# Kernel tuning notes

Measured on AMD Instinct MI355X. Metric: run time of the kernel, lower is better.

## Reference

```python
import jax, jax.numpy as jnp
import numpy as np

N_NODES = 50000
N_EDGES = 800000
D_IN = 128
D_OUT = 128
BN_EPS = 1e-5


def setup_inputs() -> dict:
    key = jax.random.key(0)
    ks = jax.random.split(key, 6)
    feat = jax.random.normal(ks[0], (N_NODES, D_IN), dtype=jnp.float32)
    src = jax.random.randint(ks[1], (N_EDGES,), 0, N_NODES, dtype=jnp.int32)
    dst = jax.random.randint(ks[2], (N_EDGES,), 0, N_NODES, dtype=jnp.int32)
    W = jax.random.normal(ks[3], (D_IN, D_OUT), dtype=jnp.float32) * (1.0 / np.sqrt(D_IN))
    b = jnp.zeros((D_OUT,), dtype=jnp.float32)
    a1 = jnp.full((1,), 0.25, dtype=jnp.float32)  # PReLU inside GraphConv
    gamma = jnp.ones((D_OUT,), dtype=jnp.float32)
    beta = jnp.zeros((D_OUT,), dtype=jnp.float32)
    a2 = jnp.full((1,), 0.25, dtype=jnp.float32)  # PReLU after BN
    return {"feat": feat, "src": src, "dst": dst, "W": W, "b": b,
            "a1": a1, "gamma": gamma, "beta": beta, "a2": a2}


def _prelu(x, a):
    return jnp.where(x >= 0, x, a * x)


def reference(feat, src, dst, W, b, a1, gamma, beta, a2):
    # Degrees (DGL clamps to min 1 to avoid inf norms)
    ones_e = jnp.ones((src.shape[0],), dtype=feat.dtype)
    out_deg = jnp.clip(jax.ops.segment_sum(ones_e, src, num_segments=N_NODES), 1.0)
    in_deg = jnp.clip(jax.ops.segment_sum(ones_e, dst, num_segments=N_NODES), 1.0)
    norm_src = jax.lax.rsqrt(out_deg)[:, None]   # [N,1]
    norm_dst = jax.lax.rsqrt(in_deg)[:, None]    # [N,1]

    # Dropout (eval mode -> identity), source normalization, projection
    h = (feat * norm_src) @ W                    # [N, D_OUT]
    # Gather-scatter neighbor aggregation (SpMM): sum over incoming edges
    msg = h[src]                                 # [E, D_OUT]
    agg = jax.ops.segment_sum(msg, dst, num_segments=N_NODES)  # [N, D_OUT]
    h = agg * norm_dst + b                       # dst normalization + bias
    h = _prelu(h, a1)                            # GraphConv activation

    # BatchNorm1d over node dimension (training-mode batch stats, biased var)
    mean = jnp.mean(h, axis=0)
    var = jnp.mean((h - mean) ** 2, axis=0)
    h = (h - mean) * jax.lax.rsqrt(var + BN_EPS) * gamma + beta

    return _prelu(h, a2)
```

## Files before the change

kernel.cpp:

```cpp
#include <hip/hip_runtime.h>
#include <hip/hip_bf16.h>

#define N_NODES 50000
#define N_EDGES 800000
#define D 128
#define BN_EPS 1e-5f
#define ELLW 64
#define PROJ_LDK 136
#define SPMM_BLOCKS 1564

#define BINS 128
#define BIN_RANGE 391
#define BINCAP 8192
#define A_EPT 13
#define A_BLOCKS 256

typedef __attribute__((ext_vector_type(8))) short bf16x8;
typedef __attribute__((ext_vector_type(4))) float f32x4;

__device__ inline float bf_lo(unsigned u) { union { unsigned x; float f; } c; c.x = u << 16; return c.f; }
__device__ inline float bf_hi(unsigned u) { union { unsigned x; float f; } c; c.x = u & 0xffff0000u; return c.f; }
__device__ inline unsigned short f2bf(float f) {
    union { float f; unsigned u; } c; c.f = f;
    unsigned u = c.u;
    u += 0x7fff + ((u >> 16) & 1);
    return (unsigned short)(u >> 16);
}
__device__ inline unsigned pack2bf(float a, float b) {
    return (unsigned)f2bf(a) | ((unsigned)f2bf(b) << 16);
}

__global__ __launch_bounds__(256) void bucket_kernel(const int* __restrict__ src,
                                                     const int* __restrict__ dst,
                                                     int* __restrict__ gdbase,
                                                     int* __restrict__ gsbase,
                                                     unsigned* __restrict__ dbkt,
                                                     unsigned short* __restrict__ sbkt) {
    __shared__ int dcnt[BINS], scnt[BINS], dbase[BINS], sbase[BINS];
    const int tid = threadIdx.x;
    if (tid < BINS) { dcnt[tid] = 0; scnt[tid] = 0; }
    __syncthreads();

    const int e0 = blockIdx.x * (256 * A_EPT) + tid;
    int s[A_EPT], t[A_EPT], dr[A_EPT], sr[A_EPT];
    #pragma unroll
    for (int k = 0; k < A_EPT; ++k) {
        int e = e0 + k * 256;
        if (e < N_EDGES) { s[k] = src[e]; t[k] = dst[e]; }
        else             { s[k] = -1;     t[k] = -1;     }
    }
    #pragma unroll
    for (int k = 0; k < A_EPT; ++k) {
        if (t[k] >= 0) dr[k] = atomicAdd(&dcnt[t[k] / BIN_RANGE], 1);
        if (s[k] >= 0) sr[k] = atomicAdd(&scnt[s[k] / BIN_RANGE], 1);
    }
    __syncthreads();
    if (tid < BINS) {
        dbase[tid] = atomicAdd(&gdbase[tid], dcnt[tid]);
        sbase[tid] = atomicAdd(&gsbase[tid], scnt[tid]);
    }
    __syncthreads();
    #pragma unroll
    for (int k = 0; k < A_EPT; ++k) {
        if (t[k] >= 0) {
            int b = t[k] / BIN_RANGE;
            int p = dbase[b] + dr[k];
            if (p < BINCAP)
                dbkt[b * BINCAP + p] = (unsigned)s[k] | ((unsigned)(t[k] - b * BIN_RANGE) << 16);
        }
        if (s[k] >= 0) {
            int b = s[k] / BIN_RANGE;
            int p = sbase[b] + sr[k];
            if (p < BINCAP)
                sbkt[b * BINCAP + p] = (unsigned short)(s[k] - b * BIN_RANGE);
        }
    }
}

__global__ __launch_bounds__(1024) void build_kernel(const int* __restrict__ gdbase,
                                                     const int* __restrict__ gsbase,
                                                     const unsigned* __restrict__ dbkt,
                                                     const unsigned short* __restrict__ sbkt,
                                                     unsigned short* __restrict__ ell,
                                                     int* __restrict__ cnt,
                                                     int* __restrict__ deg_out) {
    __shared__ int hist[BIN_RANGE];
    const int tid = threadIdx.x;
    const int bin = blockIdx.x & (BINS - 1);
    const int lo  = bin * BIN_RANGE;

    for (int i = tid; i < BIN_RANGE; i += 1024) hist[i] = 0;
    __syncthreads();

    if (blockIdx.x < BINS) {
        int count = gdbase[bin]; if (count > BINCAP) count = BINCAP;
        const unsigned* bkt = dbkt + bin * BINCAP;
        int i = tid;
        for (; i + 3072 < count; i += 4096) {
            unsigned e0 = bkt[i], e1 = bkt[i + 1024], e2 = bkt[i + 2048], e3 = bkt[i + 3072];
            int r0 = atomicAdd(&hist[e0 >> 16], 1);
            int r1 = atomicAdd(&hist[e1 >> 16], 1);
            int r2 = atomicAdd(&hist[e2 >> 16], 1);
            int r3 = atomicAdd(&hist[e3 >> 16], 1);
            if (r0 < ELLW) ell[(size_t)(lo + (e0 >> 16)) * ELLW + r0] = (unsigned short)(e0 & 0xffffu);
            if (r1 < ELLW) ell[(size_t)(lo + (e1 >> 16)) * ELLW + r1] = (unsigned short)(e1 & 0xffffu);
            if (r2 < ELLW) ell[(size_t)(lo + (e2 >> 16)) * ELLW + r2] = (unsigned short)(e2 & 0xffffu);
            if (r3 < ELLW) ell[(size_t)(lo + (e3 >> 16)) * ELLW + r3] = (unsigned short)(e3 & 0xffffu);
        }
        for (; i < count; i += 1024) {
            unsigned e = bkt[i];
            int r = atomicAdd(&hist[e >> 16], 1);
            if (r < ELLW) ell[(size_t)(lo + (e >> 16)) * ELLW + r] = (unsigned short)(e & 0xffffu);
        }
        __syncthreads();
        for (int j = tid; j < BIN_RANGE; j += 1024)
            if (lo + j < N_NODES) cnt[lo + j] = hist[j];
    } else {
        int count = gsbase[bin]; if (count > BINCAP) count = BINCAP;
        const unsigned short* bkt = sbkt + bin * BINCAP;
        int i = tid;
        for (; i + 3072 < count; i += 4096) {
            int v0 = bkt[i], v1 = bkt[i + 1024], v2 = bkt[i + 2048], v3 = bkt[i + 3072];
            atomicAdd(&hist[v0], 1); atomicAdd(&hist[v1], 1);
            atomicAdd(&hist[v2], 1); atomicAdd(&hist[v3], 1);
        }
        for (; i < count; i += 1024) atomicAdd(&hist[bkt[i]], 1);
        __syncthreads();
        for (int j = tid; j < BIN_RANGE; j += 1024)
            if (lo + j < N_NODES) deg_out[lo + j] = hist[j];
    }
}

__global__ __launch_bounds__(256, 2) void proj_kernel(const float* __restrict__ feat,
                                                      const float* __restrict__ W,
                                                      const int* __restrict__ deg_out,
                                                      unsigned short* __restrict__ h) {
    __shared__ unsigned short Wt[D * PROJ_LDK];

    const int tid  = threadIdx.x;
    const int wave = tid >> 6;
    const int lane = tid & 63;
    const int quad = lane >> 4;
    const int l16  = lane & 15;

    for (int idx = tid; idx < D * D; idx += 256) {
        int k = idx >> 7, d = idx & 127;
        Wt[d * PROJ_LDK + k] = f2bf(W[idx]);
    }
    __syncthreads();

    bf16x8 breg[8][4];
    #pragma unroll
    for (int dt = 0; dt < 8; ++dt)
        #pragma unroll
        for (int kk = 0; kk < 4; ++kk)
            breg[dt][kk] = *(const bf16x8*)&Wt[(dt * 16 + l16) * PROJ_LDK + kk * 32 + quad * 8];

    const int n_tiles = (N_NODES + 63) / 64;
    for (int tile = blockIdx.x; tile < n_tiles; tile += gridDim.x) {
        const int base = tile * 64;
        const int arow = base + wave * 16 + l16;
        const bool rok = arow < N_NODES;
        float nm;
        {
            int dg = rok ? deg_out[arow] : 1;
            nm = rsqrtf((float)(dg < 1 ? 1 : dg));
        }

        f32x4 acc[8];
        #pragma unroll
        for (int dt = 0; dt < 8; ++dt) acc[dt] = (f32x4){0.f, 0.f, 0.f, 0.f};

        #pragma unroll
        for (int kk = 0; kk < 4; ++kk) {
            bf16x8 af;
            if (rok) {
                const float4* fp = (const float4*)(feat + (size_t)arow * D + kk * 32 + quad * 8);
                float4 f0 = fp[0], f1 = fp[1];
                af[0] = (short)f2bf(f0.x * nm); af[1] = (short)f2bf(f0.y * nm);
                af[2] = (short)f2bf(f0.z * nm); af[3] = (short)f2bf(f0.w * nm);
                af[4] = (short)f2bf(f1.x * nm); af[5] = (short)f2bf(f1.y * nm);
                af[6] = (short)f2bf(f1.z * nm); af[7] = (short)f2bf(f1.w * nm);
            } else {
                af = (bf16x8){0, 0, 0, 0, 0, 0, 0, 0};
            }
            #pragma unroll
            for (int dt = 0; dt < 8; ++dt)
                acc[dt] = __builtin_amdgcn_mfma_f32_16x16x32_bf16(af, breg[dt][kk], acc[dt], 0, 0, 0);
        }

        #pragma unroll
        for (int dt = 0; dt < 8; ++dt) {
            #pragma unroll
            for (int r = 0; r < 4; ++r) {
                int n = base + wave * 16 + quad * 4 + r;
                if (n < N_NODES)
                    h[(size_t)n * D + dt * 16 + l16] = f2bf(acc[dt][r]);
            }
        }
    }
}

#define ACCA(v) { accA[0] += bf_lo((v).x); accA[1] += bf_hi((v).x); \
                  accA[2] += bf_lo((v).y); accA[3] += bf_hi((v).y); \
                  accA[4] += bf_lo((v).z); accA[5] += bf_hi((v).z); \
                  accA[6] += bf_lo((v).w); accA[7] += bf_hi((v).w); }
#define ACCB(v) { accB[0] += bf_lo((v).x); accB[1] += bf_hi((v).x); \
                  accB[2] += bf_lo((v).y); accB[3] += bf_hi((v).y); \
                  accB[4] += bf_lo((v).z); accB[5] += bf_hi((v).z); \
                  accB[6] += bf_lo((v).w); accB[7] += bf_hi((v).w); }
#define GA(sid) { uint4 vv = *(const uint4*)(h + (size_t)(sid) * D + coff); ACCA(vv); }
#define GB(sid) { uint4 vv = *(const uint4*)(h + (size_t)(sid) * D + coff); ACCB(vv); }

__global__ __launch_bounds__(256) void spmm_kernel(const int* __restrict__ cnt,
                                                   const unsigned short* __restrict__ ell,
                                                   const unsigned short* __restrict__ h,
                                                   const float* __restrict__ b,
                                                   const float* __restrict__ a1,
                                                   unsigned short* __restrict__ h2,
                                                   float* __restrict__ bn_sum,
                                                   float* __restrict__ bn_sumsq) {
    const int tid  = threadIdx.x;
    const int l16  = tid & 15;
    const int slot = (blockIdx.x * 256 + tid) >> 4;
    const float alpha = a1[0];
    const size_t coff = (size_t)l16 * 8;

    float bias[8];
    #pragma unroll
    for (int j = 0; j < 8; ++j) bias[j] = b[l16 * 8 + j];

    float lsum[8] = {0,0,0,0,0,0,0,0};
    float lsq[8]  = {0,0,0,0,0,0,0,0};

    if (slot < N_NODES / 2) {
        const int n0 = slot * 2;
        const int n1 = n0 + 1;
        int dgA = cnt[n0], dgB = cnt[n1];
        int endA = (dgA < ELLW) ? dgA : ELLW;
        int endB = (dgB < ELLW) ? dgB : ELLW;
        const unsigned short* rowA = ell + (size_t)n0 * ELLW;
        const unsigned short* rowB = ell + (size_t)n1 * ELLW;

        float accA[8] = {0,0,0,0,0,0,0,0};
        float accB[8] = {0,0,0,0,0,0,0,0};
        int iA = 0, iB = 0;

        while (iA + 8 <= endA && iB + 8 <= endB) {
            uint4 ra = *(const uint4*)(rowA + iA);
            uint4 rb = *(const uint4*)(rowB + iB);
            GA(ra.x & 0xffff); GA(ra.x >> 16);
            GA(ra.y & 0xffff); GA(ra.y >> 16);
            GA(ra.z & 0xffff); GA(ra.z >> 16);
            GA(ra.w & 0xffff); GA(ra.w >> 16);
            GB(rb.x & 0xffff); GB(rb.x >> 16);
            GB(rb.y & 0xffff); GB(rb.y >> 16);
            GB(rb.z & 0xffff); GB(rb.z >> 16);
            GB(rb.w & 0xffff); GB(rb.w >> 16);
            iA += 8; iB += 8;
        }
        for (; iA + 8 <= endA; iA += 8) {
            uint4 ra = *(const uint4*)(rowA + iA);
            GA(ra.x & 0xffff); GA(ra.x >> 16);
            GA(ra.y & 0xffff); GA(ra.y >> 16);
            GA(ra.z & 0xffff); GA(ra.z >> 16);
            GA(ra.w & 0xffff); GA(ra.w >> 16);
        }
        for (; iB + 8 <= endB; iB += 8) {
            uint4 rb = *(const uint4*)(rowB + iB);
            GB(rb.x & 0xffff); GB(rb.x >> 16);
            GB(rb.y & 0xffff); GB(rb.y >> 16);
            GB(rb.z & 0xffff); GB(rb.z >> 16);
            GB(rb.w & 0xffff); GB(rb.w >> 16);
        }
        for (; iA < endA; ++iA) { GA(rowA[iA]); }
        for (; iB < endB; ++iB) { GB(rowB[iB]); }

        float ndA = rsqrtf((float)(dgA < 1 ? 1 : dgA));
        float ndB = rsqrtf((float)(dgB < 1 ? 1 : dgB));
        float xA[8], xB[8];
        #pragma unroll
        for (int j = 0; j < 8; ++j) {
            float va = accA[j] * ndA + bias[j];
            va = (va >= 0.f) ? va : alpha * va;
            xA[j] = va; lsum[j] += va; lsq[j] += va * va;
            float vb = accB[j] * ndB + bias[j];
            vb = (vb >= 0.f) ? vb : alpha * vb;
            xB[j] = vb; lsum[j] += vb; lsq[j] += vb * vb;
        }
        uint4 oA, oB;
        oA.x = pack2bf(xA[0], xA[1]); oA.y = pack2bf(xA[2], xA[3]);
        oA.z = pack2bf(xA[4], xA[5]); oA.w = pack2bf(xA[6], xA[7]);
        oB.x = pack2bf(xB[0], xB[1]); oB.y = pack2bf(xB[2], xB[3]);
        oB.z = pack2bf(xB[4], xB[5]); oB.w = pack2bf(xB[6], xB[7]);
        *(uint4*)(h2 + (size_t)n0 * D + coff) = oA;
        *(uint4*)(h2 + (size_t)n1 * D + coff) = oB;
    }

    #pragma unroll
    for (int j = 0; j < 8; ++j) {
        lsum[j] += __shfl_xor(lsum[j], 16);
        lsum[j] += __shfl_xor(lsum[j], 32);
        lsq[j]  += __shfl_xor(lsq[j], 16);
        lsq[j]  += __shfl_xor(lsq[j], 32);
    }
    __shared__ float red[4][256];
    const int wave = tid >> 6;
    const int lane = tid & 63;
    if (lane < 16) {
        #pragma unroll
        for (int j = 0; j < 8; ++j) {
            red[wave][l16 * 16 + j]     = lsum[j];
            red[wave][l16 * 16 + 8 + j] = lsq[j];
        }
    }
    __syncthreads();
    {
        float tot = red[0][tid] + red[1][tid] + red[2][tid] + red[3][tid];
        int l = tid >> 4;
        int v = tid & 15;
        int dim = l * 8 + (v & 7);
        int rep = (blockIdx.x & 3) * D;
        if (v < 8) atomicAdd(&bn_sum[rep + dim], tot);
        else       atomicAdd(&bn_sumsq[rep + dim], tot);
    }
}

__global__ __launch_bounds__(256) void final_kernel(const unsigned short* __restrict__ h2,
                                                    const float* __restrict__ bn_sum,
                                                    const float* __restrict__ bn_sumsq,
                                                    const float* __restrict__ gamma,
                                                    const float* __restrict__ beta,
                                                    const float* __restrict__ a2,
                                                    float* __restrict__ out) {
    int i8 = blockIdx.x * 256 + threadIdx.x;
    if (i8 < N_NODES * D / 8) {
        int dbase = (i8 * 8) & (D - 1);
        const float invN = 1.0f / (float)N_NODES;
        const float alpha = a2[0];
        uint4 v = ((const uint4*)h2)[i8];
        float xv[8] = { bf_lo(v.x), bf_hi(v.x), bf_lo(v.y), bf_hi(v.y),
                        bf_lo(v.z), bf_hi(v.z), bf_lo(v.w), bf_hi(v.w) };
        float r[8];
        #pragma unroll
        for (int j = 0; j < 8; ++j) {
            int d = dbase + j;
            float sm = bn_sum[d] + bn_sum[D + d] + bn_sum[2 * D + d] + bn_sum[3 * D + d];
            float sq = bn_sumsq[d] + bn_sumsq[D + d] + bn_sumsq[2 * D + d] + bn_sumsq[3 * D + d];
            float mean = sm * invN;
            float var  = sq * invN - mean * mean;
            float inv  = rsqrtf(var + BN_EPS);
            float t = (xv[j] - mean) * inv * gamma[d] + beta[d];
            r[j] = (t >= 0.f) ? t : alpha * t;
        }
        float4* po = (float4*)(out + (size_t)i8 * 8);
        po[0] = make_float4(r[0], r[1], r[2], r[3]);
        po[1] = make_float4(r[4], r[5], r[6], r[7]);
    }
}

extern "C" void kernel_launch(void* const* d_in, const int* in_sizes, int n_in,
                              void* d_out, int out_size, void* d_ws, size_t ws_size,
                              hipStream_t stream) {
    const float* feat  = (const float*)d_in[0];
    const int*   src   = (const int*)  d_in[1];
    const int*   dst   = (const int*)  d_in[2];
    const float* W     = (const float*)d_in[3];
    const float* b     = (const float*)d_in[4];
    const float* a1    = (const float*)d_in[5];
    const float* gamma = (const float*)d_in[6];
    const float* beta  = (const float*)d_in[7];
    const float* a2    = (const float*)d_in[8];
    float* out = (float*)d_out;

    char* ws = (char*)d_ws;
    int*            gdbase    = (int*)(ws + 0);
    int*            gsbase    = (int*)(ws + 512);
    float*          bn_sum    = (float*)(ws + 1024);
    float*          bn_sumsq  = (float*)(ws + 3072);
    int*            cnt       = (int*)(ws + 5120);
    int*            deg_out_p = (int*)(ws + 205120);
    unsigned short* ell       = (unsigned short*)(ws + 405120);
    unsigned short* h         = (unsigned short*)(ws + 6805120);
    unsigned short* h2        = (unsigned short*)(ws + 19605120);
    unsigned*       dbkt      = (unsigned*)(ws + 32405120);
    unsigned short* sbkt      = (unsigned short*)(ws + 36599424);

    hipMemsetAsync(ws, 0, 5120, stream);

    bucket_kernel<<<A_BLOCKS, 256, 0, stream>>>(src, dst, gdbase, gsbase, dbkt, sbkt);

    build_kernel<<<2 * BINS, 1024, 0, stream>>>(gdbase, gsbase, dbkt, sbkt,
                                                ell, cnt, deg_out_p);

    proj_kernel<<<782, 256, 0, stream>>>(feat, W, deg_out_p, h);

    spmm_kernel<<<SPMM_BLOCKS, 256, 0, stream>>>(cnt, ell, h, b, a1, h2, bn_sum, bn_sumsq);

    final_kernel<<<(N_NODES * D / 8 + 255) / 256, 256, 0, stream>>>(h2, bn_sum, bn_sumsq,
                                                                    gamma, beta, a2, out);
}
```

Baseline: 183.2 us.

## Fuse projection into bucketing kernel and apply source norm inside SpMM gather

The projection no longer needs out-degrees, because the per-source normalization is now applied as a scalar per gathered row inside the SpMM. That lets the projection GEMM run in the same launch as edge bucketing, with extra blocks handling the projection tiles, which removes one kernel launch and lets the two independent stages overlap. build_kernel now writes rsqrt(out-degree) floats instead of raw degree ints. Software bf16 rounding is replaced with the v_cvt_pk_bf16_f32 instruction. In exchange, the SpMM does an extra scalar load per edge, feat is converted to bf16 before scaling, which changes rounding slightly, and each projection block now restages W for only a single tile.

```diff
diff --git a/kernel.cpp b/kernel.cpp
--- a/kernel.cpp
+++ b/kernel.cpp
@@ -8,6 +8,7 @@
 #define ELLW 64
 #define PROJ_LDK 136
 #define SPMM_BLOCKS 1564
+#define PROJ_TILES 782
 
 #define BINS 128
 #define BIN_RANGE 391
@@ -26,53 +27,125 @@
     u += 0x7fff + ((u >> 16) & 1);
     return (unsigned short)(u >> 16);
 }
-__device__ inline unsigned pack2bf(float a, float b) {
-    return (unsigned)f2bf(a) | ((unsigned)f2bf(b) << 16);
-}
-
-__global__ __launch_bounds__(256) void bucket_kernel(const int* __restrict__ src,
-                                                     const int* __restrict__ dst,
-                                                     int* __restrict__ gdbase,
-                                                     int* __restrict__ gsbase,
-                                                     unsigned* __restrict__ dbkt,
-                                                     unsigned short* __restrict__ sbkt) {
+__device__ inline unsigned cvt_pk_bf16(float lo, float hi) {
+    unsigned r;
+    asm("v_cvt_pk_bf16_f32 %0, %1, %2" : "=v"(r) : "v"(lo), "v"(hi));
+    return r;
+}
+
+__global__ __launch_bounds__(256, 2) void bucket_proj_kernel(
+        const int* __restrict__ src,
+        const int* __restrict__ dst,
+        int* __restrict__ gdbase,
+        int* __restrict__ gsbase,
+        unsigned* __restrict__ dbkt,
+        unsigned short* __restrict__ sbkt,
+        const float* __restrict__ feat,
+        const float* __restrict__ W,
+        unsigned short* __restrict__ h) {
     __shared__ int dcnt[BINS], scnt[BINS], dbase[BINS], sbase[BINS];
+    __shared__ unsigned short Wt[D * PROJ_LDK];
+
     const int tid = threadIdx.x;
-    if (tid < BINS) { dcnt[tid] = 0; scnt[tid] = 0; }
-    __syncthreads();
-
-    const int e0 = blockIdx.x * (256 * A_EPT) + tid;
-    int s[A_EPT], t[A_EPT], dr[A_EPT], sr[A_EPT];
-    #pragma unroll
-    for (int k = 0; k < A_EPT; ++k) {
-        int e = e0 + k * 256;
-        if (e < N_EDGES) { s[k] = src[e]; t[k] = dst[e]; }
-        else             { s[k] = -1;     t[k] = -1;     }
-    }
-    #pragma unroll
-    for (int k = 0; k < A_EPT; ++k) {
-        if (t[k] >= 0) dr[k] = atomicAdd(&dcnt[t[k] / BIN_RANGE], 1);
-        if (s[k] >= 0) sr[k] = atomicAdd(&scnt[s[k] / BIN_RANGE], 1);
-    }
-    __syncthreads();
-    if (tid < BINS) {
-        dbase[tid] = atomicAdd(&gdbase[tid], dcnt[tid]);
-        sbase[tid] = atomicAdd(&gsbase[tid], scnt[tid]);
-    }
-    __syncthreads();
-    #pragma unroll
-    for (int k = 0; k < A_EPT; ++k) {
-        if (t[k] >= 0) {
-            int b = t[k] / BIN_RANGE;
-            int p = dbase[b] + dr[k];
-            if (p < BINCAP)
-                dbkt[b * BINCAP + p] = (unsigned)s[k] | ((unsigned)(t[k] - b * BIN_RANGE) << 16);
-        }
-        if (s[k] >= 0) {
-            int b = s[k] / BIN_RANGE;
-            int p = sbase[b] + sr[k];
-            if (p < BINCAP)
-                sbkt[b * BINCAP + p] = (unsigned short)(s[k] - b * BIN_RANGE);
+
+    if (blockIdx.x < A_BLOCKS) {
+        if (tid < BINS) { dcnt[tid] = 0; scnt[tid] = 0; }
+        __syncthreads();
+
+        const int e0 = blockIdx.x * (256 * A_EPT) + tid;
+        int s[A_EPT], t[A_EPT], dr[A_EPT], sr[A_EPT];
+        #pragma unroll
+        for (int k = 0; k < A_EPT; ++k) {
+            int e = e0 + k * 256;
+            if (e < N_EDGES) { s[k] = src[e]; t[k] = dst[e]; }
+            else             { s[k] = -1;     t[k] = -1;     }
+        }
+        #pragma unroll
+        for (int k = 0; k < A_EPT; ++k) {
+            if (t[k] >= 0) dr[k] = atomicAdd(&dcnt[t[k] / BIN_RANGE], 1);
+            if (s[k] >= 0) sr[k] = atomicAdd(&scnt[s[k] / BIN_RANGE], 1);
+        }
+        __syncthreads();
+        if (tid < BINS) {
+            dbase[tid] = atomicAdd(&gdbase[tid], dcnt[tid]);
+            sbase[tid] = atomicAdd(&gsbase[tid], scnt[tid]);
+        }
+        __syncthreads();
+        #pragma unroll
+        for (int k = 0; k < A_EPT; ++k) {
+            if (t[k] >= 0) {
+                int bb = t[k] / BIN_RANGE;
+                int p = dbase[bb] + dr[k];
+                if (p < BINCAP)
+                    dbkt[bb * BINCAP + p] = (unsigned)s[k] | ((unsigned)(t[k] - bb * BIN_RANGE) << 16);
+            }
+            if (s[k] >= 0) {
+                int bb = s[k] / BIN_RANGE;
+                int p = sbase[bb] + sr[k];
+                if (p < BINCAP)
+                    sbkt[bb * BINCAP + p] = (unsigned short)(s[k] - bb * BIN_RANGE);
+            }
+        }
+    } else {
+        const int tile = blockIdx.x - A_BLOCKS;
+        const int wave = tid >> 6;
+        const int lane = tid & 63;
+        const int quad = lane >> 4;
+        const int l16  = lane & 15;
+
+        for (int idx = tid; idx < D * D; idx += 256) {
+            int k = idx >> 7, d = idx & 127;
+            Wt[d * PROJ_LDK + k] = f2bf(W[idx]);
+        }
+        __syncthreads();
+
+        bf16x8 breg[8][4];
+        #pragma unroll
+        for (int dt = 0; dt < 8; ++dt)
+            #pragma unroll
+            for (int kk = 0; kk < 4; ++kk)
+                breg[dt][kk] = *(const bf16x8*)&Wt[(dt * 16 + l16) * PROJ_LDK + kk * 32 + quad * 8];
+
+        const int base = tile * 64;
+        const int arow = base + wave * 16 + l16;
+        const bool rok = arow < N_NODES;
+
+        f32x4 acc[8];
+        #pragma unroll
+        for (int dt = 0; dt < 8; ++dt) acc[dt] = (f32x4){0.f, 0.f, 0.f, 0.f};
+
+        #pragma unroll
+        for (int kk = 0; kk < 4; ++kk) {
+            bf16x8 af = (bf16x8){0, 0, 0, 0, 0, 0, 0, 0};
+            if (rok) {
+                const float4* fp = (const float4*)(feat + (size_t)arow * D + kk * 32 + quad * 8);
+                float4 f0 = fp[0], f1 = fp[1];
+                unsigned u0 = cvt_pk_bf16(f0.x, f0.y);
+                unsigned u1 = cvt_pk_bf16(f0.z, f0.w);
+                unsigned u2 = cvt_pk_bf16(f1.x, f1.y);
+                unsigned u3 = cvt_pk_bf16(f1.z, f1.w);
+                af[0] = (short)(u0 & 0xffff); af[1] = (short)(u0 >> 16);
+                af[2] = (short)(u1 & 0xffff); af[3] = (short)(u1 >> 16);
+                af[4] = (short)(u2 & 0xffff); af[5] = (short)(u2 >> 16);
+                af[6] = (short)(u3 & 0xffff); af[7] = (short)(u3 >> 16);
+            }
+            #pragma unroll
+            for (int dt = 0; dt < 8; ++dt)
+                acc[dt] = __builtin_amdgcn_mfma_f32_16x16x32_bf16(af, breg[dt][kk], acc[dt], 0, 0, 0);
+        }
+
+        #pragma unroll
+        for (int r = 0; r < 4; ++r) {
+            int n = base + wave * 16 + quad * 4 + r;
+            if (n < N_NODES) {
+                unsigned short* hp = h + (size_t)n * D + l16;
+                #pragma unroll
+                for (int dt = 0; dt < 8; dt += 2) {
+                    unsigned pk = cvt_pk_bf16(acc[dt][r], acc[dt + 1][r]);
+                    hp[dt * 16]       = (unsigned short)(pk & 0xffff);
+                    hp[(dt + 1) * 16] = (unsigned short)(pk >> 16);
+                }
+            }
         }
     }
 }
@@ -83,7 +156,7 @@
                                                      const unsigned short* __restrict__ sbkt,
                                                      unsigned short* __restrict__ ell,
                                                      int* __restrict__ cnt,
-                                                     int* __restrict__ deg_out) {
+                                                     float* __restrict__ nsrc) {
     __shared__ int hist[BIN_RANGE];
     const int tid = threadIdx.x;
     const int bin = blockIdx.x & (BINS - 1);
@@ -127,92 +200,28 @@
         for (; i < count; i += 1024) atomicAdd(&hist[bkt[i]], 1);
         __syncthreads();
         for (int j = tid; j < BIN_RANGE; j += 1024)
-            if (lo + j < N_NODES) deg_out[lo + j] = hist[j];
-    }
-}
-
-__global__ __launch_bounds__(256, 2) void proj_kernel(const float* __restrict__ feat,
-                                                      const float* __restrict__ W,
-                                                      const int* __restrict__ deg_out,
-                                                      unsigned short* __restrict__ h) {
-    __shared__ unsigned short Wt[D * PROJ_LDK];
-
-    const int tid  = threadIdx.x;
-    const int wave = tid >> 6;
-    const int lane = tid & 63;
-    const int quad = lane >> 4;
-    const int l16  = lane & 15;
-
-    for (int idx = tid; idx < D * D; idx += 256) {
-        int k = idx >> 7, d = idx & 127;
-        Wt[d * PROJ_LDK + k] = f2bf(W[idx]);
-    }
-    __syncthreads();
-
-    bf16x8 breg[8][4];
-    #pragma unroll
-    for (int dt = 0; dt < 8; ++dt)
-        #pragma unroll
-        for (int kk = 0; kk < 4; ++kk)
-            breg[dt][kk] = *(const bf16x8*)&Wt[(dt * 16 + l16) * PROJ_LDK + kk * 32 + quad * 8];
-
-    const int n_tiles = (N_NODES + 63) / 64;
-    for (int tile = blockIdx.x; tile < n_tiles; tile += gridDim.x) {
-        const int base = tile * 64;
-        const int arow = base + wave * 16 + l16;
-        const bool rok = arow < N_NODES;
-        float nm;
-        {
-            int dg = rok ? deg_out[arow] : 1;
-            nm = rsqrtf((float)(dg < 1 ? 1 : dg));
-        }
-
-        f32x4 acc[8];
-        #pragma unroll
-        for (int dt = 0; dt < 8; ++dt) acc[dt] = (f32x4){0.f, 0.f, 0.f, 0.f};
-
-        #pragma unroll
-        for (int kk = 0; kk < 4; ++kk) {
-            bf16x8 af;
-            if (rok) {
-                const float4* fp = (const float4*)(feat + (size_t)arow * D + kk * 32 + quad * 8);
-                float4 f0 = fp[0], f1 = fp[1];
-                af[0] = (short)f2bf(f0.x * nm); af[1] = (short)f2bf(f0.y * nm);
-                af[2] = (short)f2bf(f0.z * nm); af[3] = (short)f2bf(f0.w * nm);
-                af[4] = (short)f2bf(f1.x * nm); af[5] = (short)f2bf(f1.y * nm);
-                af[6] = (short)f2bf(f1.z * nm); af[7] = (short)f2bf(f1.w * nm);
-            } else {
-                af = (bf16x8){0, 0, 0, 0, 0, 0, 0, 0};
+            if (lo + j < N_NODES) {
+                int dg = hist[j];
+                nsrc[lo + j] = rsqrtf((float)(dg < 1 ? 1 : dg));
             }
-            #pragma unroll
-            for (int dt = 0; dt < 8; ++dt)
-                acc[dt] = __builtin_amdgcn_mfma_f32_16x16x32_bf16(af, breg[dt][kk], acc[dt], 0, 0, 0);
-        }
-
-        #pragma unroll
-        for (int dt = 0; dt < 8; ++dt) {
-            #pragma unroll
-            for (int r = 0; r < 4; ++r) {
-                int n = base + wave * 16 + quad * 4 + r;
-                if (n < N_NODES)
-                    h[(size_t)n * D + dt * 16 + l16] = f2bf(acc[dt][r]);
-            }
-        }
-    }
-}
-
-#define ACCA(v) { accA[0] += bf_lo((v).x); accA[1] += bf_hi((v).x); \
-                  accA[2] += bf_lo((v).y); accA[3] += bf_hi((v).y); \
-                  accA[4] += bf_lo((v).z); accA[5] += bf_hi((v).z); \
-                  accA[6] += bf_lo((v).w); accA[7] += bf_hi((v).w); }
-#define ACCB(v) { accB[0] += bf_lo((v).x); accB[1] += bf_hi((v).x); \
-                  accB[2] += bf_lo((v).y); accB[3] += bf_hi((v).y); \
-                  accB[4] += bf_lo((v).z); accB[5] += bf_hi((v).z); \
-                  accB[6] += bf_lo((v).w); accB[7] += bf_hi((v).w); }
-#define GA(sid) { uint4 vv = *(const uint4*)(h + (size_t)(sid) * D + coff); ACCA(vv); }
-#define GB(sid) { uint4 vv = *(const uint4*)(h + (size_t)(sid) * D + coff); ACCB(vv); }
+    }
+}
+
+#define ACCA(v, ns) { accA[0] = fmaf(bf_lo((v).x), ns, accA[0]); accA[1] = fmaf(bf_hi((v).x), ns, accA[1]); \
+                      accA[2] = fmaf(bf_lo((v).y), ns, accA[2]); accA[3] = fmaf(bf_hi((v).y), ns, accA[3]); \
+                      accA[4] = fmaf(bf_lo((v).z), ns, accA[4]); accA[5] = fmaf(bf_hi((v).z), ns, accA[5]); \
+                      accA[6] = fmaf(bf_lo((v).w), ns, accA[6]); accA[7] = fmaf(bf_hi((v).w), ns, accA[7]); }
+#define ACCB(v, ns) { accB[0] = fmaf(bf_lo((v).x), ns, accB[0]); accB[1] = fmaf(bf_hi((v).x), ns, accB[1]); \
+                      accB[2] = fmaf(bf_lo((v).y), ns, accB[2]); accB[3] = fmaf(bf_hi((v).y), ns, accB[3]); \
+                      accB[4] = fmaf(bf_lo((v).z), ns, accB[4]); accB[5] = fmaf(bf_hi((v).z), ns, accB[5]); \
+                      accB[6] = fmaf(bf_lo((v).w), ns, accB[6]); accB[7] = fmaf(bf_hi((v).w), ns, accB[7]); }
+#define GA(sid) { int _s = (int)(sid); uint4 vv = *(const uint4*)(h + (size_t)_s * D + coff); \
+                  float ns = nsrc[_s]; ACCA(vv, ns); }
+#define GB(sid) { int _s = (int)(sid); uint4 vv = *(const uint4*)(h + (size_t)_s * D + coff); \
+                  float ns = nsrc[_s]; ACCB(vv, ns); }
 
 __global__ __launch_bounds__(256) void spmm_kernel(const int* __restrict__ cnt,
+                                                   const float* __restrict__ nsrc,
                                                    const unsigned short* __restrict__ ell,
                                                    const unsigned short* __restrict__ h,
                                                    const float* __restrict__ b,
@@ -289,10 +298,10 @@
             xB[j] = vb; lsum[j] += vb; lsq[j] += vb * vb;
         }
         uint4 oA, oB;
-        oA.x = pack2bf(xA[0], xA[1]); oA.y = pack2bf(xA[2], xA[3]);
-        oA.z = pack2bf(xA[4], xA[5]); oA.w = pack2bf(xA[6], xA[7]);
-        oB.x = pack2bf(xB[0], xB[1]); oB.y = pack2bf(xB[2], xB[3]);
-        oB.z = pack2bf(xB[4], xB[5]); oB.w = pack2bf(xB[6], xB[7]);
+        oA.x = cvt_pk_bf16(xA[0], xA[1]); oA.y = cvt_pk_bf16(xA[2], xA[3]);
+        oA.z = cvt_pk_bf16(xA[4], xA[5]); oA.w = cvt_pk_bf16(xA[6], xA[7]);
+        oB.x = cvt_pk_bf16(xB[0], xB[1]); oB.y = cvt_pk_bf16(xB[2], xB[3]);
+        oB.z = cvt_pk_bf16(xB[4], xB[5]); oB.w = cvt_pk_bf16(xB[6], xB[7]);
         *(uint4*)(h2 + (size_t)n0 * D + coff) = oA;
         *(uint4*)(h2 + (size_t)n1 * D + coff) = oB;
     }
@@ -379,7 +388,7 @@
     float*          bn_sum    = (float*)(ws + 1024);
     float*          bn_sumsq  = (float*)(ws + 3072);
     int*            cnt       = (int*)(ws + 5120);
-    int*            deg_out_p = (int*)(ws + 205120);
+    float*          nsrc      = (float*)(ws + 205120);
     unsigned short* ell       = (unsigned short*)(ws + 405120);
     unsigned short* h         = (unsigned short*)(ws + 6805120);
     unsigned short* h2        = (unsigned short*)(ws + 19605120);
@@ -388,14 +397,14 @@
 
     hipMemsetAsync(ws, 0, 5120, stream);
 
-    bucket_kernel<<<A_BLOCKS, 256, 0, stream>>>(src, dst, gdbase, gsbase, dbkt, sbkt);
+    bucket_proj_kernel<<<A_BLOCKS + PROJ_TILES, 256, 0, stream>>>(
+        src, dst, gdbase, gsbase, dbkt, sbkt, feat, W, h);
 
     build_kernel<<<2 * BINS, 1024, 0, stream>>>(gdbase, gsbase, dbkt, sbkt,
-                                                ell, cnt, deg_out_p);
-
-    proj_kernel<<<782, 256, 0, stream>>>(feat, W, deg_out_p, h);
-
-    spmm_kernel<<<SPMM_BLOCKS, 256, 0, stream>>>(cnt, ell, h, b, a1, h2, bn_sum, bn_sumsq);
+                                                ell, cnt, nsrc);
+
+    spmm_kernel<<<SPMM_BLOCKS, 256, 0, stream>>>(cnt, nsrc, ell, h, b, a1, h2,
+                                                 bn_sum, bn_sumsq);
 
     final_kernel<<<(N_NODES * D / 8 + 255) / 256, 256, 0, stream>>>(h2, bn_sum, bn_sumsq,
                                                                     gamma, beta, a2, out);
```

New measurement: 179.8 us. About the same (-1.9%).
